# Kernel optimization log

Hardware: AMD Instinct MI355X
Metric: run time of the kernel (lower is better)

Reference implementation:

```python
import jax, jax.numpy as jnp
import numpy as np

B, N, D_MODEL, LAP = 64, 64, 256, 16


def setup_inputs() -> dict:
    key = jax.random.key(0)
    ks = jax.random.split(key, 8)
    adj = jax.random.randint(ks[0], (B, N, N), 0, 2, dtype=jnp.int32)
    node_feats = jax.random.normal(ks[1], (B, N, D_MODEL), dtype=jnp.float32)
    eigvec = jax.random.normal(ks[2], (B, N, LAP), dtype=jnp.float32)
    W_lap = jax.random.normal(ks[3], (LAP, D_MODEL), dtype=jnp.float32) / np.sqrt(LAP)
    W_edge = jax.random.normal(ks[4], (1 + 2 * LAP, D_MODEL), dtype=jnp.float32) / np.sqrt(1 + 2 * LAP)
    b_edge = jax.random.normal(ks[5], (D_MODEL,), dtype=jnp.float32) * 0.02
    type_embed = jax.random.normal(ks[6], (2, D_MODEL), dtype=jnp.float32)
    graph_tok = jax.random.normal(ks[7], (1, 1, D_MODEL), dtype=jnp.float32)
    return {"adj": adj, "node_feats": node_feats, "eigvec": eigvec,
            "W_lap": W_lap, "W_edge": W_edge, "b_edge": b_edge,
            "type_embed": type_embed, "graph_tok": graph_tok}


def reference(adj, node_feats, eigvec, W_lap, W_edge, b_edge, type_embed, graph_tok):
    b, n, _ = adj.shape
    d = graph_tok.shape[-1]
    # node tokens: feats + LapPE projection
    node_tok = node_feats + jnp.einsum('bnl,ld->bnd', eigvec, W_lap)
    # upper-triangular candidate edges (fixed M = n(n-1)/2, jit-friendly)
    iu, ju = jnp.triu_indices(n, k=1)               # [M]
    valid = adj[:, iu, ju] > 0                       # [B, M]
    # stable compaction: valid edges first (matches torch per-graph extraction order)
    order = jnp.argsort(~valid, axis=1, stable=True) # [B, M]
    src = iu[order]                                  # [B, M]
    dst = ju[order]
    valid_sorted = jnp.take_along_axis(valid, order, axis=1)
    Pu = jnp.take_along_axis(eigvec, src[..., None], axis=1)  # [B, M, LAP]
    Pv = jnp.take_along_axis(eigvec, dst[..., None], axis=1)
    m = src.shape[1]
    edge_in = jnp.concatenate([jnp.ones((b, m, 1), eigvec.dtype), Pu, Pv], axis=-1)
    etok = jnp.einsum('bmf,fd->bmd', edge_in, W_edge) + b_edge + type_embed[1]
    etok = jnp.where(valid_sorted[..., None], etok, 0.0)      # zeros at padding
    pad_mask_edges = ~valid_sorted                             # True = padding
    gtok = jnp.broadcast_to(graph_tok, (b, 1, d))
    seq_embeds = jnp.concatenate([gtok, node_tok, etok], axis=1)  # [B, 1+n+M, d]
    pad_mask = jnp.concatenate([jnp.zeros((b, 1 + n), bool), pad_mask_edges], axis=1)
    return seq_embeds, pad_mask
```

## Files before the change

### kernel.cpp

```cpp
#include <hip/hip_runtime.h>

#define B_ 64
#define N_ 64
#define D_ 256
#define LAP_ 16
#define M_ 2016
#define TOK_ 2081

__global__ __launch_bounds__(256) void compact_kernel(const int* __restrict__ adj,
                                                      int* __restrict__ pack) {
    int b = blockIdx.x;
    int t = threadIdx.x;
    __shared__ int s[256];
    __shared__ int s_total;

    int ii[8], jj[8], vv[8];
    int c = 0;
#pragma unroll
    for (int k = 0; k < 8; k++) {
        int m = t * 8 + k;
        int valid = 0, i = 0, j = 0;
        if (m < M_) {
            float fm = (float)m;
            int gi = (int)((127.0f - sqrtf(127.0f * 127.0f - 8.0f * fm)) * 0.5f);
            if (gi < 0) gi = 0;
            if (gi > 62) gi = 62;
            while (gi > 0 && (127 * gi - gi * gi) / 2 > m) gi--;
            while (gi < 62 && (127 * (gi + 1) - (gi + 1) * (gi + 1)) / 2 <= m) gi++;
            i = gi;
            j = i + 1 + (m - (127 * i - i * i) / 2);
            valid = (adj[b * (N_ * N_) + i * N_ + j] > 0) ? 1 : 0;
        }
        ii[k] = i; jj[k] = j; vv[k] = valid;
        c += valid;
    }
    s[t] = c;
    __syncthreads();
    for (int off = 1; off < 256; off <<= 1) {
        int v = (t >= off) ? s[t - off] : 0;
        __syncthreads();
        s[t] += v;
        __syncthreads();
    }
    if (t == 255) s_total = s[255];
    __syncthreads();
    int total = s_total;
    int run = s[t] - c;
#pragma unroll
    for (int k = 0; k < 8; k++) {
        int m = t * 8 + k;
        if (m < M_) {
            int p;
            if (vv[k]) { p = run; run++; }
            else       { p = total + (m - run); }
            pack[b * M_ + p] = ii[k] | (jj[k] << 8) | (vv[k] << 16);
        }
    }
}

__global__ __launch_bounds__(256) void head_kernel(const float* __restrict__ graph_tok,
                                                   float* __restrict__ out) {
    int b = blockIdx.x;
    int t = threadIdx.x;
    out[(size_t)b * TOK_ * D_ + t] = graph_tok[t];
    float* mask = out + (size_t)B_ * TOK_ * D_;
    if (t < 1 + N_) mask[b * TOK_ + t] = 0.0f;
}

__global__ __launch_bounds__(256) void node_kernel(const float* __restrict__ node_feats,
                                                   const float* __restrict__ eigvec,
                                                   const float* __restrict__ W_lap,
                                                   float* __restrict__ out) {
    int b = blockIdx.x;
    int n = blockIdx.y * 4 + (threadIdx.x >> 6);
    int lane = threadIdx.x & 63;
    const float* e = eigvec + (size_t)(b * N_ + n) * LAP_;
    float4 acc = ((const float4*)(node_feats + ((size_t)b * N_ + n) * D_))[lane];
#pragma unroll
    for (int l = 0; l < LAP_; l++) {
        float el = e[l];
        float4 w = ((const float4*)(W_lap + l * D_))[lane];
        acc.x += el * w.x; acc.y += el * w.y; acc.z += el * w.z; acc.w += el * w.w;
    }
    ((float4*)(out + (size_t)b * TOK_ * D_ + (size_t)(1 + n) * D_))[lane] = acc;
}

__global__ __launch_bounds__(256) void edge_kernel(const float* __restrict__ eigvec,
                                                   const float* __restrict__ W_edge,
                                                   const float* __restrict__ b_edge,
                                                   const float* __restrict__ type_embed,
                                                   const int* __restrict__ pack,
                                                   float* __restrict__ out) {
    __shared__ float sW[32 * D_];
    __shared__ float sBase[D_];
    __shared__ float sEig[N_ * LAP_];

    int b = blockIdx.x;
    int t = threadIdx.x;

    sBase[t] = W_edge[t] + b_edge[t] + type_embed[D_ + t];
    {
        const float4* src = (const float4*)(W_edge + D_);
        float4* dst = (float4*)sW;
#pragma unroll
        for (int k = 0; k < 8; k++) dst[t + 256 * k] = src[t + 256 * k];
        ((float4*)sEig)[t] = ((const float4*)(eigvec + (size_t)b * N_ * LAP_))[t];
    }
    __syncthreads();

    int wave = t >> 6, lane = t & 63;
    float* maskb = out + (size_t)B_ * TOK_ * D_ + (size_t)b * TOK_ + 1 + N_;
    float* outb = out + (size_t)b * TOK_ * D_ + (size_t)(1 + N_) * D_;

#pragma unroll
    for (int k = 0; k < 8; k++) {
        int p = blockIdx.y * 32 + wave * 8 + k;
        int pk = pack[b * M_ + p];
        float4 acc = make_float4(0.f, 0.f, 0.f, 0.f);
        int valid = (pk >> 16) & 1;
        if (valid) {
            int si = pk & 0xff, di = (pk >> 8) & 0xff;
            const float* eu = sEig + si * LAP_;
            const float* ev = sEig + di * LAP_;
            acc = ((float4*)sBase)[lane];
#pragma unroll
            for (int l = 0; l < LAP_; l++) {
                float pu = eu[l], pv = ev[l];
                float4 w1 = ((float4*)(sW + l * D_))[lane];
                float4 w2 = ((float4*)(sW + (LAP_ + l) * D_))[lane];
                acc.x += pu * w1.x + pv * w2.x;
                acc.y += pu * w1.y + pv * w2.y;
                acc.z += pu * w1.z + pv * w2.z;
                acc.w += pu * w1.w + pv * w2.w;
            }
        }
        ((float4*)(outb + (size_t)p * D_))[lane] = acc;
        if (lane == 0) maskb[p] = valid ? 0.0f : 1.0f;
    }
}

extern "C" void kernel_launch(void* const* d_in, const int* in_sizes, int n_in,
                              void* d_out, int out_size, void* d_ws, size_t ws_size,
                              hipStream_t stream) {
    const int*   adj        = (const int*)d_in[0];
    const float* node_feats = (const float*)d_in[1];
    const float* eigvec     = (const float*)d_in[2];
    const float* W_lap      = (const float*)d_in[3];
    const float* W_edge     = (const float*)d_in[4];
    const float* b_edge     = (const float*)d_in[5];
    const float* type_embed = (const float*)d_in[6];
    const float* graph_tok  = (const float*)d_in[7];
    float* out = (float*)d_out;
    int* pack = (int*)d_ws;

    compact_kernel<<<dim3(B_), dim3(256), 0, stream>>>(adj, pack);
    head_kernel<<<dim3(B_), dim3(256), 0, stream>>>(graph_tok, out);
    node_kernel<<<dim3(B_, 16), dim3(256), 0, stream>>>(node_feats, eigvec, W_lap, out);
    edge_kernel<<<dim3(B_, 63), dim3(256), 0, stream>>>(eigvec, W_edge, b_edge,
                                                        type_embed, pack, out);
}
```

Measured before the change: 181.2 us.

## Hold edge weights in registers and fold head kernel into node kernel

The edge kernel no longer stages the 32x256 weight matrix and base vector in shared memory. Each lane now loads its float4 slice of all 32 weight rows into registers and reads the eigenvector rows as float4. This cuts the 33 KB shared-memory footprint per block, which limited occupancy, at the cost of about 128 extra VGPRs per thread. The separate head kernel is merged into the node kernel's blockIdx.y==0 blocks, saving one launch.

```diff
diff --git a/kernel.cpp b/kernel.cpp
--- a/kernel.cpp
+++ b/kernel.cpp
@@ -58,22 +58,15 @@
     }
 }
 
-__global__ __launch_bounds__(256) void head_kernel(const float* __restrict__ graph_tok,
+__global__ __launch_bounds__(256) void node_kernel(const float* __restrict__ node_feats,
+                                                   const float* __restrict__ eigvec,
+                                                   const float* __restrict__ W_lap,
+                                                   const float* __restrict__ graph_tok,
                                                    float* __restrict__ out) {
     int b = blockIdx.x;
     int t = threadIdx.x;
-    out[(size_t)b * TOK_ * D_ + t] = graph_tok[t];
-    float* mask = out + (size_t)B_ * TOK_ * D_;
-    if (t < 1 + N_) mask[b * TOK_ + t] = 0.0f;
-}
-
-__global__ __launch_bounds__(256) void node_kernel(const float* __restrict__ node_feats,
-                                                   const float* __restrict__ eigvec,
-                                                   const float* __restrict__ W_lap,
-                                                   float* __restrict__ out) {
-    int b = blockIdx.x;
-    int n = blockIdx.y * 4 + (threadIdx.x >> 6);
-    int lane = threadIdx.x & 63;
+    int n = blockIdx.y * 4 + (t >> 6);
+    int lane = t & 63;
     const float* e = eigvec + (size_t)(b * N_ + n) * LAP_;
     float4 acc = ((const float4*)(node_feats + ((size_t)b * N_ + n) * D_))[lane];
 #pragma unroll
@@ -83,6 +76,12 @@
         acc.x += el * w.x; acc.y += el * w.y; acc.z += el * w.z; acc.w += el * w.w;
     }
     ((float4*)(out + (size_t)b * TOK_ * D_ + (size_t)(1 + n) * D_))[lane] = acc;
+
+    if (blockIdx.y == 0) {
+        out[(size_t)b * TOK_ * D_ + t] = graph_tok[t];
+        float* mask = out + (size_t)B_ * TOK_ * D_;
+        if (t < 1 + N_) mask[b * TOK_ + t] = 0.0f;
+    }
 }
 
 __global__ __launch_bounds__(256) void edge_kernel(const float* __restrict__ eigvec,
@@ -91,24 +90,29 @@
                                                    const float* __restrict__ type_embed,
                                                    const int* __restrict__ pack,
                                                    float* __restrict__ out) {
-    __shared__ float sW[32 * D_];
-    __shared__ float sBase[D_];
     __shared__ float sEig[N_ * LAP_];
 
     int b = blockIdx.x;
     int t = threadIdx.x;
+    int wave = t >> 6, lane = t & 63;
 
-    sBase[t] = W_edge[t] + b_edge[t] + type_embed[D_ + t];
+    ((float4*)sEig)[t] = ((const float4*)(eigvec + (size_t)b * N_ * LAP_))[t];
+
+    float4 base = ((const float4*)W_edge)[lane];
     {
-        const float4* src = (const float4*)(W_edge + D_);
-        float4* dst = (float4*)sW;
+        float4 bb = ((const float4*)b_edge)[lane];
+        float4 te = ((const float4*)(type_embed + D_))[lane];
+        base.x += bb.x + te.x; base.y += bb.y + te.y;
+        base.z += bb.z + te.z; base.w += bb.w + te.w;
+    }
+    float4 w1[LAP_], w2[LAP_];
 #pragma unroll
-        for (int k = 0; k < 8; k++) dst[t + 256 * k] = src[t + 256 * k];
-        ((float4*)sEig)[t] = ((const float4*)(eigvec + (size_t)b * N_ * LAP_))[t];
+    for (int l = 0; l < LAP_; l++) {
+        w1[l] = ((const float4*)(W_edge + (1 + l) * D_))[lane];
+        w2[l] = ((const float4*)(W_edge + (1 + LAP_ + l) * D_))[lane];
     }
     __syncthreads();
 
-    int wave = t >> 6, lane = t & 63;
     float* maskb = out + (size_t)B_ * TOK_ * D_ + (size_t)b * TOK_ + 1 + N_;
     float* outb = out + (size_t)b * TOK_ * D_ + (size_t)(1 + N_) * D_;
 
@@ -120,18 +124,21 @@
         int valid = (pk >> 16) & 1;
         if (valid) {
             int si = pk & 0xff, di = (pk >> 8) & 0xff;
-            const float* eu = sEig + si * LAP_;
-            const float* ev = sEig + di * LAP_;
-            acc = ((float4*)sBase)[lane];
+            const float4* eu4 = (const float4*)(sEig + si * LAP_);
+            const float4* ev4 = (const float4*)(sEig + di * LAP_);
+            float4 eu[4], ev[4];
+#pragma unroll
+            for (int q = 0; q < 4; q++) { eu[q] = eu4[q]; ev[q] = ev4[q]; }
+            acc = base;
+            const float* euf = (const float*)eu;
+            const float* evf = (const float*)ev;
 #pragma unroll
             for (int l = 0; l < LAP_; l++) {
-                float pu = eu[l], pv = ev[l];
-                float4 w1 = ((float4*)(sW + l * D_))[lane];
-                float4 w2 = ((float4*)(sW + (LAP_ + l) * D_))[lane];
-                acc.x += pu * w1.x + pv * w2.x;
-                acc.y += pu * w1.y + pv * w2.y;
-                acc.z += pu * w1.z + pv * w2.z;
-                acc.w += pu * w1.w + pv * w2.w;
+                float pu = euf[l], pv = evf[l];
+                acc.x += pu * w1[l].x + pv * w2[l].x;
+                acc.y += pu * w1[l].y + pv * w2[l].y;
+                acc.z += pu * w1[l].z + pv * w2[l].z;
+                acc.w += pu * w1[l].w + pv * w2[l].w;
             }
         }
         ((float4*)(outb + (size_t)p * D_))[lane] = acc;
@@ -154,8 +161,8 @@
     int* pack = (int*)d_ws;
 
     compact_kernel<<<dim3(B_), dim3(256), 0, stream>>>(adj, pack);
-    head_kernel<<<dim3(B_), dim3(256), 0, stream>>>(graph_tok, out);
-    node_kernel<<<dim3(B_, 16), dim3(256), 0, stream>>>(node_feats, eigvec, W_lap, out);
+    node_kernel<<<dim3(B_, 16), dim3(256), 0, stream>>>(node_feats, eigvec, W_lap,
+                                                        graph_tok, out);
     edge_kernel<<<dim3(B_, 63), dim3(256), 0, stream>>>(eigvec, W_edge, b_edge,
                                                         type_embed, pack, out);
 }
```

New measurement: 179.5 us. About the same (-0.9%).
